# Performance work log

Measured on AMD Instinct MI355X. Metric: run time of the kernel, lower is better.

## Reference

```python
import jax, jax.numpy as jnp
import numpy as np

G, T, H, E, F, C = 8, 2048, 512, 8, 2048, 256


def setup_inputs() -> dict:
    key = jax.random.key(0)
    ks = jax.random.split(key, 4)
    s = 0.02  # truncated-normal stddev in the original init (plain normal here)
    return {
        "x": jax.random.normal(ks[0], (G, T, H), jnp.float32),
        "router_kernel": jax.random.normal(ks[1], (H, E), jnp.float32) * s,
        "router_bias": jnp.zeros((E,), jnp.float32),
        "wi": jax.random.normal(ks[2], (E, H, F), jnp.float32) * s,
        "bi": jnp.zeros((E, F), jnp.float32),
        "wo": jax.random.normal(ks[3], (E, F, H), jnp.float32) * s,
        "bo": jnp.zeros((E, H), jnp.float32),
        "expert_capacity": C,
    }


def reference(x, router_kernel, router_bias, wi, bi, wo, bo, expert_capacity):
    # ---- Router (eval mode: no jitter noise, no dropout) ----
    # logits / probs: [g, t, e]
    router_logits = jnp.einsum("gth,he->gte", x, router_kernel) + router_bias
    router_probs = jax.nn.softmax(router_logits, axis=-1)

    # Experts-choose masked routing: each expert picks its top-capacity tokens.
    probs_et = jnp.swapaxes(router_probs, 1, 2)              # [g, e, t]
    expert_gate, expert_index = jax.lax.top_k(probs_et, expert_capacity)  # [g, e, c]
    dispatch = jax.nn.one_hot(expert_index, x.shape[1], dtype=x.dtype)    # [g, e, c, t]
    combine = dispatch * expert_gate[..., None]                            # [g, e, c, t]

    # ---- Dispatch: gather tokens into per-expert buffers ----
    expert_inputs = jnp.einsum("gect,gth->gech", dispatch, x)  # [g, e, c, h]

    # ---- Per-expert FFN (batched einsum GEMMs) ----
    h_mid = jax.nn.gelu(
        jnp.einsum("gech,ehf->gecf", expert_inputs, wi) + bi[None, :, None, :],
        approximate=False,
    )
    expert_out = jnp.einsum("gecf,efh->gech", h_mid, wo) + bo[None, :, None, :]

    # ---- Combine: scatter expert outputs back, scaled by router prob ----
    y = jnp.einsum("gect,gech->gth", combine, expert_out)  # [g, t, h]
    return y
```

## Files before the change

kernel.cpp:

```cpp
#include <hip/hip_runtime.h>
#include <cstdint>
#include <cstddef>

#define G_ 8
#define T_ 2048
#define H_ 512
#define E_ 8
#define F_ 2048
#define C_ 256

typedef __bf16 bf16x8 __attribute__((ext_vector_type(8)));
typedef float f32x4 __attribute__((ext_vector_type(4)));

__device__ __forceinline__ unsigned short f2bf(float f) {
  unsigned u = __float_as_uint(f);
  u += 0x7FFFu + ((u >> 16) & 1u);
  return (unsigned short)(u >> 16);
}

__device__ __forceinline__ void gload_lds16(const void* g, void* l) {
  __builtin_amdgcn_global_load_lds(
      (const __attribute__((address_space(1))) void*)g,
      (__attribute__((address_space(3))) void*)l, 16, 0, 0);
}

__device__ __forceinline__ float fast_gelu(float v) {
  float z = v * (1.5957691216f + 0.0713540727f * v * v);
  float e = __expf(-z);
  return v * __builtin_amdgcn_rcpf(1.0f + e);
}

#define BARRIER() do { __builtin_amdgcn_s_barrier(); asm volatile("" ::: "memory"); } while (0)

__global__ __launch_bounds__(256) void transconv_kernel(const float* __restrict__ in,
                                 unsigned short* __restrict__ out,
                                 int R, int Cc, int tC) {
  __shared__ float tile[64][65];
  int tid = threadIdx.x;
  int nT = (R / 64) * tC;
  int b = blockIdx.x / nT;
  int rem = blockIdx.x % nT;
  int tr = rem / tC, tc = rem % tC;
  const float* ib = in + (size_t)b * R * Cc + (size_t)(tr * 64) * Cc + tc * 64;
  unsigned short* ob = out + (size_t)b * R * Cc;
  int lr = tid >> 4, lc = (tid & 15) * 4;
#pragma unroll
  for (int i = 0; i < 4; ++i) {
    float4 v = *(const float4*)&ib[(size_t)(lr + 16 * i) * Cc + lc];
    tile[lr + 16 * i][lc + 0] = v.x;
    tile[lr + 16 * i][lc + 1] = v.y;
    tile[lr + 16 * i][lc + 2] = v.z;
    tile[lr + 16 * i][lc + 3] = v.w;
  }
  __syncthreads();
  int r = (tid & 31) * 2, c0 = tid >> 5;
#pragma unroll
  for (int i = 0; i < 8; ++i) {
    int c = c0 + i * 8;
    ushort2 o;
    o.x = f2bf(tile[r][c]);
    o.y = f2bf(tile[r + 1][c]);
    *(ushort2*)&ob[(size_t)(tc * 64 + c) * R + tr * 64 + r] = o;
  }
}

__global__ void router_kernel(const float* __restrict__ x, const float* __restrict__ rk,
                              const float* __restrict__ rb, float* __restrict__ probs) {
  __shared__ float rks[H_ * E_];
  int tid = threadIdx.x;
  for (int i = tid; i < H_ * E_ / 4; i += 256)
    ((float4*)rks)[i] = ((const float4*)rk)[i];
  __syncthreads();
  int wid = tid >> 6, lane = tid & 63;
  int row = blockIdx.x * 4 + wid;
  float acc[E_];
#pragma unroll
  for (int e = 0; e < E_; ++e) acc[e] = 0.f;
  const float* xr = x + (size_t)row * H_;
#pragma unroll
  for (int j = 0; j < H_ / 64; ++j) {
    int h = j * 64 + lane;
    float xv = xr[h];
    const float4* r4 = (const float4*)&rks[h * E_];
    float4 r0 = r4[0], r1 = r4[1];
    acc[0] += xv * r0.x; acc[1] += xv * r0.y; acc[2] += xv * r0.z; acc[3] += xv * r0.w;
    acc[4] += xv * r1.x; acc[5] += xv * r1.y; acc[6] += xv * r1.z; acc[7] += xv * r1.w;
  }
#pragma unroll
  for (int e = 0; e < E_; ++e) {
#pragma unroll
    for (int off = 32; off > 0; off >>= 1) acc[e] += __shfl_xor(acc[e], off);
  }
  float l[E_];
  float mx = -1e30f;
#pragma unroll
  for (int e = 0; e < E_; ++e) { l[e] = acc[e] + rb[e]; mx = fmaxf(mx, l[e]); }
  float s = 0.f;
#pragma unroll
  for (int e = 0; e < E_; ++e) { l[e] = expf(l[e] - mx); s += l[e]; }
  float inv = 1.0f / s;
  int g = row >> 11, t = row & (T_ - 1);
  if (lane < E_) probs[((size_t)(g * E_ + lane)) * T_ + t] = l[lane] * inv;
}

__global__ __launch_bounds__(1024) void topk_kernel(const float* __restrict__ probs,
                                                    int* __restrict__ idx,
                                                    float* __restrict__ gate) {
  __shared__ unsigned long long keys[T_];
  int ge = blockIdx.x, tid = threadIdx.x;
  const float* p = probs + (size_t)ge * T_;
#pragma unroll
  for (int j = 0; j < 2; ++j) {
    int t = tid + j * 1024;
    unsigned pb = __float_as_uint(p[t]);
    keys[t] = ((unsigned long long)pb << 32) | (unsigned)(~t);
  }
  __syncthreads();
  for (unsigned k = 2; k <= T_; k <<= 1) {
    for (unsigned j = k >> 1; j > 0; j >>= 1) {
      unsigned w = tid;
      unsigned i = ((w & ~(j - 1)) << 1) | (w & (j - 1));
      unsigned q = i + j;
      unsigned long long a = keys[i], b = keys[q];
      bool sw = ((i & k) == 0) ? (a < b) : (a > b);
      if (sw) { keys[i] = b; keys[q] = a; }
      __syncthreads();
    }
  }
  if (tid < C_) {
    unsigned long long kk = keys[tid];
    gate[ge * C_ + tid] = __uint_as_float((unsigned)(kk >> 32));
    idx[ge * C_ + tid] = (int)(~(unsigned)kk);
  }
}

__global__ void gather_kernel(const float* __restrict__ x, const int* __restrict__ idx,
                              unsigned short* __restrict__ xin) {
  int tid = threadIdx.x, wid = tid >> 6, lane = tid & 63;
  int r = blockIdx.x * 4 + wid;
  int ge = r >> 8;
  int g = ge >> 3;
  int t = idx[r];
  const float* src = x + ((size_t)(g * T_ + t)) * H_;
  unsigned short* dst = xin + (size_t)r * H_;
#pragma unroll
  for (int j = 0; j < 2; ++j) {
    int h = j * 256 + lane * 4;
    float4 v = *(const float4*)&src[h];
    ushort4 o;
    o.x = f2bf(v.x); o.y = f2bf(v.y); o.z = f2bf(v.z); o.w = f2bf(v.w);
    *(ushort4*)&dst[h] = o;
  }
}

__global__ void build_kernel(const int* __restrict__ idx, int* __restrict__ cnt,
                             unsigned short* __restrict__ ent) {
  int id = blockIdx.x * 256 + threadIdx.x;
  int ge = id >> 8, c = id & 255;
  int g = ge >> 3, e = ge & 7;
  int t = idx[id];
  int pos = atomicAdd(&cnt[g * T_ + t], 1);
  ent[(g * T_ + t) * 8 + pos] = (unsigned short)((e << 8) | c);
}

__global__ __launch_bounds__(256) void combine_kernel(const unsigned short* __restrict__ eout,
                                                      const int* __restrict__ cnt,
                                                      const unsigned short* __restrict__ ent,
                                                      const float* __restrict__ gate,
                                                      float* __restrict__ y) {
  int tid = threadIdx.x, wid = tid >> 6, lane = tid & 63;
  int row = blockIdx.x * 4 + wid;
  int g = row >> 11;
  int n = cnt[row];
  float a[8] = {0.f, 0.f, 0.f, 0.f, 0.f, 0.f, 0.f, 0.f};
  for (int i = 0; i < n; ++i) {
    unsigned pe = ent[row * 8 + i];
    int e = pe >> 8, c = pe & 255;
    int ge = g * E_ + e;
    float gv = gate[ge * C_ + c];
    bf16x8 v = *(const bf16x8*)&eout[((size_t)ge * C_ + c) * H_ + lane * 8];
#pragma unroll
    for (int j = 0; j < 8; ++j) a[j] += gv * (float)v[j];
  }
  float* yr = y + (size_t)row * H_ + lane * 8;
  *(float4*)yr = make_float4(a[0], a[1], a[2], a[3]);
  *(float4*)(yr + 4) = make_float4(a[4], a[5], a[6], a[7]);
}

template<int NT>
__device__ __forceinline__ void gemm_core(const unsigned short* __restrict__ Abase,
                                          const unsigned short* __restrict__ Bbase,
                                          int ldK, unsigned short* lds,
                                          f32x4 (&acc)[8][4]) {
  int tid = threadIdx.x;
  int wid = tid >> 6, lane = tid & 63;
  int l15 = lane & 15, g4 = lane >> 4;
  int wm = wid >> 2, wn = wid & 3;

  int off0, off1;
  {
    int ob = tid * 16;
    int lr = ob >> 7, b = ((ob >> 4) & 7) ^ (lr & 7);
    off0 = (2 * lr + (b >> 2)) * ldK + (b & 3) * 8;
    ob = 8192 + tid * 16;
    lr = ob >> 7; b = ((ob >> 4) & 7) ^ (lr & 7);
    off1 = (2 * lr + (b >> 2)) * ldK + (b & 3) * 8;
  }
  int blkphys = (((l15 & 1) << 2) | g4) ^ (l15 >> 1);
  int abase = (wm * 64 + (l15 >> 1)) * 64 + blkphys * 8;
  int bbase = 8192 + (wn * 32 + (l15 >> 1)) * 64 + blkphys * 8;

  auto stage = [&](int kt) {
    unsigned short* sb = lds + (kt & 3) * 16384;
    const unsigned short* ga = Abase + kt * 32;
    const unsigned short* gb = Bbase + kt * 32;
    gload_lds16(ga + off0, sb + wid * 512);
    gload_lds16(ga + off1, sb + 4096 + wid * 512);
    gload_lds16(gb + off0, sb + 8192 + wid * 512);
    gload_lds16(gb + off1, sb + 12288 + wid * 512);
  };

  auto compute = [&](int kt) {
    const unsigned short* sb = lds + (kt & 3) * 16384;
    bf16x8 af[8], bfr[4];
#pragma unroll
    for (int m = 0; m < 8; ++m) af[m] = *(const bf16x8*)&sb[abase + m * 512];
#pragma unroll
    for (int n = 0; n < 4; ++n) bfr[n] = *(const bf16x8*)&sb[bbase + n * 512];
    __builtin_amdgcn_s_setprio(1);
#pragma unroll
    for (int m = 0; m < 8; ++m)
#pragma unroll
      for (int n = 0; n < 4; ++n)
        acc[m][n] = __builtin_amdgcn_mfma_f32_16x16x32_bf16(af[m], bfr[n], acc[m][n], 0, 0, 0);
    __builtin_amdgcn_s_setprio(0);
  };

  stage(0); stage(1); stage(2);
  asm volatile("s_waitcnt vmcnt(8)" ::: "memory");
  BARRIER();
  for (int kt = 0; kt < NT - 3; ++kt) {
    stage(kt + 3);
    compute(kt);
    asm volatile("s_waitcnt vmcnt(8)" ::: "memory");
    BARRIER();
  }
  compute(NT - 3);
  asm volatile("s_waitcnt vmcnt(4)" ::: "memory");
  BARRIER();
  compute(NT - 2);
  asm volatile("s_waitcnt vmcnt(0)" ::: "memory");
  BARRIER();
  compute(NT - 1);
}

__global__ __launch_bounds__(512, 2) void gemm1_kernel(const unsigned short* __restrict__ xin,
                                                       const unsigned short* __restrict__ wiT,
                                                       const float* __restrict__ bi,
                                                       unsigned short* __restrict__ hmid) {
  __shared__ unsigned short lds[65536];
  int bid = blockIdx.x;
  int swz = (bid & 7) * 64 + (bid >> 3);
  int e = swz >> 6, rem = swz & 63, nt = rem >> 3, g = rem & 7;
  int ge = g * E_ + e;
  const unsigned short* Abase = xin + (size_t)ge * C_ * H_;
  const unsigned short* Bbase = wiT + (size_t)e * F_ * H_ + (size_t)(nt * 256) * H_;
  f32x4 acc[8][4] = {};
  gemm_core<H_ / 32>(Abase, Bbase, H_, lds, acc);

  int tid = threadIdx.x, wid = tid >> 6, lane = tid & 63;
  int l15 = lane & 15, g4 = lane >> 4, wm = wid >> 2, wn = wid & 3;
  unsigned short* Cb = hmid + (size_t)ge * C_ * F_;
  int row0 = wm * 128, col0 = nt * 256 + wn * 64;
#pragma unroll
  for (int m = 0; m < 8; ++m) {
#pragma unroll
    for (int n = 0; n < 4; ++n) {
      int col = col0 + n * 16 + l15;
      float bv = bi[e * F_ + col];
#pragma unroll
      for (int r = 0; r < 4; ++r) {
        int row = row0 + m * 16 + g4 * 4 + r;
        Cb[(size_t)row * F_ + col] = f2bf(fast_gelu(acc[m][n][r] + bv));
      }
    }
  }
}

template<int NT>
__device__ __forceinline__ void gemm2_core(const unsigned short* __restrict__ Abase,
                                           const unsigned short* __restrict__ Bbase,
                                           int ldK, unsigned short* lds,
                                           f32x4 (&acc)[8][4]) {
  int tid = threadIdx.x;
  int wid = tid >> 6, lane = tid & 63;
  int l15 = lane & 15, g4 = lane >> 4;
  int wn = wid;

  auto mkoff = [&](int ob) {
    int lr = ob >> 7, b = ((ob >> 4) & 7) ^ (lr & 7);
    return (2 * lr + (b >> 2)) * ldK + (b & 3) * 8;
  };
  int offA0 = mkoff(tid * 16), offA1 = mkoff(4096 + tid * 16);
  int offB0 = mkoff(tid * 16), offB1 = mkoff(4096 + tid * 16);
  int offB2 = mkoff(8192 + tid * 16), offB3 = mkoff(12288 + tid * 16);

  int blkphys = (((l15 & 1) << 2) | g4) ^ (l15 >> 1);
  int abase = (l15 >> 1) * 64 + blkphys * 8;
  int bbase = 4096 + (wn * 32 + (l15 >> 1)) * 64 + blkphys * 8;

  auto stage = [&](int kt, int slot) {
    unsigned short* sb = lds + slot * 12288;
    const unsigned short* ga = Abase + kt * 32;
    const unsigned short* gb = Bbase + kt * 32;
    gload_lds16(ga + offA0, sb + wid * 512);
    gload_lds16(ga + offA1, sb + 2048 + wid * 512);
    gload_lds16(gb + offB0, sb + 4096 + wid * 512);
    gload_lds16(gb + offB1, sb + 6144 + wid * 512);
    gload_lds16(gb + offB2, sb + 8192 + wid * 512);
    gload_lds16(gb + offB3, sb + 10240 + wid * 512);
  };

  auto compute = [&](int slot) {
    const unsigned short* sb = lds + slot * 12288;
    bf16x8 af[8], bfr[4];
#pragma unroll
    for (int m = 0; m < 8; ++m) af[m] = *(const bf16x8*)&sb[abase + m * 512];
#pragma unroll
    for (int n = 0; n < 4; ++n) bfr[n] = *(const bf16x8*)&sb[bbase + n * 512];
    __builtin_amdgcn_s_setprio(1);
#pragma unroll
    for (int m = 0; m < 8; ++m)
#pragma unroll
      for (int n = 0; n < 4; ++n)
        acc[m][n] = __builtin_amdgcn_mfma_f32_16x16x32_bf16(af[m], bfr[n], acc[m][n], 0, 0, 0);
    __builtin_amdgcn_s_setprio(0);
  };

  stage(0, 0); stage(1, 1);
  asm volatile("s_waitcnt vmcnt(6)" ::: "memory");
  BARRIER();
  int s0 = 0, s1 = 1, s2 = 2;
  for (int kt = 0; kt < NT - 2; ++kt) {
    stage(kt + 2, s2);
    compute(s0);
    asm volatile("s_waitcnt vmcnt(6)" ::: "memory");
    BARRIER();
    int t = s0; s0 = s1; s1 = s2; s2 = t;
  }
  compute(s0);
  asm volatile("s_waitcnt vmcnt(0)" ::: "memory");
  BARRIER();
  compute(s1);
}

__global__ __launch_bounds__(256, 2) void gemm2_kernel(const unsigned short* __restrict__ hmid,
                                                       const unsigned short* __restrict__ woT,
                                                       const float* __restrict__ bo,
                                                       unsigned short* __restrict__ eout) {
  __shared__ unsigned short lds[36864];
  int bid = blockIdx.x;
  int swz = (bid & 7) * 32 + (bid >> 3);
  int e = swz >> 5, rem = swz & 31;
  int tile = rem >> 3, g = rem & 7;
  int tm = tile >> 1, tn = tile & 1;
  int ge = g * E_ + e;
  const unsigned short* Abase = hmid + (size_t)ge * C_ * F_ + (size_t)(tm * 128) * F_;
  const unsigned short* Bbase = woT + (size_t)e * H_ * F_ + (size_t)(tn * 256) * F_;
  f32x4 acc[8][4] = {};
  gemm2_core<F_ / 32>(Abase, Bbase, F_, lds, acc);

  int tid = threadIdx.x, wid = tid >> 6, lane = tid & 63;
  int l15 = lane & 15, g4 = lane >> 4, wn = wid;
  unsigned short* Ob = eout + (size_t)ge * C_ * H_;
  int row0 = tm * 128, col0 = tn * 256 + wn * 64;
#pragma unroll
  for (int m = 0; m < 8; ++m) {
#pragma unroll
    for (int n = 0; n < 4; ++n) {
      int col = col0 + n * 16 + l15;
      float bv = bo[e * H_ + col];
#pragma unroll
      for (int r = 0; r < 4; ++r) {
        int row = row0 + m * 16 + g4 * 4 + r;
        Ob[(size_t)row * H_ + col] = f2bf(acc[m][n][r] + bv);
      }
    }
  }
}

extern "C" void kernel_launch(void* const* d_in, const int* in_sizes, int n_in,
                              void* d_out, int out_size, void* d_ws, size_t ws_size,
                              hipStream_t stream) {
  const float* x  = (const float*)d_in[0];
  const float* rk = (const float*)d_in[1];
  const float* rb = (const float*)d_in[2];
  const float* wi = (const float*)d_in[3];
  const float* bi = (const float*)d_in[4];
  const float* wo = (const float*)d_in[5];
  const float* bo = (const float*)d_in[6];
  float* y = (float*)d_out;

  const size_t WI_T = 0;
  const size_t WO_T = 16777216;
  const size_t PROB = 33554432;
  const size_t IDXO = 34078720;
  const size_t GATO = 34144256;
  const size_t XINO = 34209792;
  const size_t HMID = 50987008;
  const size_t NEED = 118095872;
  if (ws_size < NEED) return;

  char* ws = (char*)d_ws;
  unsigned short* wiT = (unsigned short*)(ws + WI_T);
  unsigned short* woT = (unsigned short*)(ws + WO_T);
  float* probs = (float*)(ws + PROB);
  int* cnt = (int*)(ws + PROB);
  unsigned short* ent = (unsigned short*)(ws + PROB + 65536);
  int* idx = (int*)(ws + IDXO);
  float* gate = (float*)(ws + GATO);
  unsigned short* xin = (unsigned short*)(ws + XINO);
  unsigned short* eout = (unsigned short*)(ws + XINO);
  unsigned short* hmid = (unsigned short*)(ws + HMID);

  transconv_kernel<<<E_ * (H_ / 64) * (F_ / 64), 256, 0, stream>>>(wi, wiT, H_, F_, F_ / 64);
  transconv_kernel<<<E_ * (F_ / 64) * (H_ / 64), 256, 0, stream>>>(wo, woT, F_, H_, H_ / 64);
  router_kernel<<<G_ * T_ / 4, 256, 0, stream>>>(x, rk, rb, probs);
  topk_kernel<<<G_ * E_, 1024, 0, stream>>>(probs, idx, gate);
  hipMemsetAsync(cnt, 0, G_ * T_ * sizeof(int), stream);
  build_kernel<<<G_ * E_ * C_ / 256, 256, 0, stream>>>(idx, cnt, ent);
  gather_kernel<<<G_ * E_ * C_ / 4, 256, 0, stream>>>(x, idx, xin);
  gemm1_kernel<<<512, 512, 0, stream>>>(xin, wiT, bi, hmid);
  gemm2_kernel<<<256, 256, 0, stream>>>(hmid, woT, bo, eout);
  combine_kernel<<<G_ * T_ / 4, 256, 0, stream>>>(eout, cnt, ent, gate, y);
}
```

Before: 167.7 us.

## Fuse prep kernels and split GEMM k-steps into half-tile MFMA phases

Merges the two weight-transpose kernels and the router into one launch, and merges gather with the dispatch-table build into another, which cuts kernel launch and tail overhead. Both GEMM cores now split each k-step into two halves of four M-fragments. The A and B global-to-LDS prefetches are interleaved between the halves, with extra barriers and LDS waits. This is meant to lower register pressure and overlap loads with MFMA, at the cost of more barriers per k-step.

```diff
diff --git a/kernel.cpp b/kernel.cpp
--- a/kernel.cpp
+++ b/kernel.cpp
@@ -31,15 +31,17 @@
 }
 
 #define BARRIER() do { __builtin_amdgcn_s_barrier(); asm volatile("" ::: "memory"); } while (0)
-
-__global__ __launch_bounds__(256) void transconv_kernel(const float* __restrict__ in,
-                                 unsigned short* __restrict__ out,
-                                 int R, int Cc, int tC) {
-  __shared__ float tile[64][65];
+#define WAIT_LDS() do { asm volatile("s_waitcnt lgkmcnt(0)" ::: "memory"); \
+                        __builtin_amdgcn_sched_barrier(0); } while (0)
+
+__device__ __forceinline__ void transconv_body(const float* __restrict__ in,
+                                               unsigned short* __restrict__ out,
+                                               int R, int Cc, int tC, int bidrem,
+                                               float* smem) {
   int tid = threadIdx.x;
   int nT = (R / 64) * tC;
-  int b = blockIdx.x / nT;
-  int rem = blockIdx.x % nT;
+  int b = bidrem / nT;
+  int rem = bidrem % nT;
   int tr = rem / tC, tc = rem % tC;
   const float* ib = in + (size_t)b * R * Cc + (size_t)(tr * 64) * Cc + tc * 64;
   unsigned short* ob = out + (size_t)b * R * Cc;
@@ -47,10 +49,10 @@
 #pragma unroll
   for (int i = 0; i < 4; ++i) {
     float4 v = *(const float4*)&ib[(size_t)(lr + 16 * i) * Cc + lc];
-    tile[lr + 16 * i][lc + 0] = v.x;
-    tile[lr + 16 * i][lc + 1] = v.y;
-    tile[lr + 16 * i][lc + 2] = v.z;
-    tile[lr + 16 * i][lc + 3] = v.w;
+    smem[(lr + 16 * i) * 65 + lc + 0] = v.x;
+    smem[(lr + 16 * i) * 65 + lc + 1] = v.y;
+    smem[(lr + 16 * i) * 65 + lc + 2] = v.z;
+    smem[(lr + 16 * i) * 65 + lc + 3] = v.w;
   }
   __syncthreads();
   int r = (tid & 31) * 2, c0 = tid >> 5;
@@ -58,21 +60,23 @@
   for (int i = 0; i < 8; ++i) {
     int c = c0 + i * 8;
     ushort2 o;
-    o.x = f2bf(tile[r][c]);
-    o.y = f2bf(tile[r + 1][c]);
+    o.x = f2bf(smem[r * 65 + c]);
+    o.y = f2bf(smem[(r + 1) * 65 + c]);
     *(ushort2*)&ob[(size_t)(tc * 64 + c) * R + tr * 64 + r] = o;
   }
 }
 
-__global__ void router_kernel(const float* __restrict__ x, const float* __restrict__ rk,
-                              const float* __restrict__ rb, float* __restrict__ probs) {
-  __shared__ float rks[H_ * E_];
+__device__ __forceinline__ void router_body(const float* __restrict__ x,
+                                            const float* __restrict__ rk,
+                                            const float* __restrict__ rb,
+                                            float* __restrict__ probs,
+                                            int bidrem, float* rks) {
   int tid = threadIdx.x;
   for (int i = tid; i < H_ * E_ / 4; i += 256)
     ((float4*)rks)[i] = ((const float4*)rk)[i];
   __syncthreads();
   int wid = tid >> 6, lane = tid & 63;
-  int row = blockIdx.x * 4 + wid;
+  int row = bidrem * 4 + wid;
   float acc[E_];
 #pragma unroll
   for (int e = 0; e < E_; ++e) acc[e] = 0.f;
@@ -101,6 +105,25 @@
   float inv = 1.0f / s;
   int g = row >> 11, t = row & (T_ - 1);
   if (lane < E_) probs[((size_t)(g * E_ + lane)) * T_ + t] = l[lane] * inv;
+}
+
+__global__ __launch_bounds__(256) void fused1_kernel(const float* __restrict__ wi,
+                                                     unsigned short* __restrict__ wiT,
+                                                     const float* __restrict__ wo,
+                                                     unsigned short* __restrict__ woT,
+                                                     const float* __restrict__ x,
+                                                     const float* __restrict__ rk,
+                                                     const float* __restrict__ rb,
+                                                     float* __restrict__ probs) {
+  __shared__ float smem[64 * 65];
+  int bid = blockIdx.x;
+  if (bid < 2048) {
+    transconv_body(wi, wiT, H_, F_, F_ / 64, bid, smem);
+  } else if (bid < 4096) {
+    transconv_body(wo, woT, F_, H_, H_ / 64, bid - 2048, smem);
+  } else {
+    router_body(x, rk, rb, probs, bid - 4096, smem);
+  }
 }
 
 __global__ __launch_bounds__(1024) void topk_kernel(const float* __restrict__ probs,
@@ -134,33 +157,36 @@
   }
 }
 
-__global__ void gather_kernel(const float* __restrict__ x, const int* __restrict__ idx,
-                              unsigned short* __restrict__ xin) {
-  int tid = threadIdx.x, wid = tid >> 6, lane = tid & 63;
-  int r = blockIdx.x * 4 + wid;
-  int ge = r >> 8;
-  int g = ge >> 3;
-  int t = idx[r];
-  const float* src = x + ((size_t)(g * T_ + t)) * H_;
-  unsigned short* dst = xin + (size_t)r * H_;
-#pragma unroll
-  for (int j = 0; j < 2; ++j) {
-    int h = j * 256 + lane * 4;
-    float4 v = *(const float4*)&src[h];
-    ushort4 o;
-    o.x = f2bf(v.x); o.y = f2bf(v.y); o.z = f2bf(v.z); o.w = f2bf(v.w);
-    *(ushort4*)&dst[h] = o;
-  }
-}
-
-__global__ void build_kernel(const int* __restrict__ idx, int* __restrict__ cnt,
-                             unsigned short* __restrict__ ent) {
-  int id = blockIdx.x * 256 + threadIdx.x;
-  int ge = id >> 8, c = id & 255;
-  int g = ge >> 3, e = ge & 7;
-  int t = idx[id];
-  int pos = atomicAdd(&cnt[g * T_ + t], 1);
-  ent[(g * T_ + t) * 8 + pos] = (unsigned short)((e << 8) | c);
+__global__ __launch_bounds__(256) void fused2_kernel(const float* __restrict__ x,
+                                                     const int* __restrict__ idx,
+                                                     unsigned short* __restrict__ xin,
+                                                     int* __restrict__ cnt,
+                                                     unsigned short* __restrict__ ent) {
+  int bid = blockIdx.x, tid = threadIdx.x;
+  if (bid < 4096) {
+    int wid = tid >> 6, lane = tid & 63;
+    int r = bid * 4 + wid;
+    int ge = r >> 8;
+    int g = ge >> 3;
+    int t = idx[r];
+    const float* src = x + ((size_t)(g * T_ + t)) * H_;
+    unsigned short* dst = xin + (size_t)r * H_;
+#pragma unroll
+    for (int j = 0; j < 2; ++j) {
+      int h = j * 256 + lane * 4;
+      float4 v = *(const float4*)&src[h];
+      ushort4 o;
+      o.x = f2bf(v.x); o.y = f2bf(v.y); o.z = f2bf(v.z); o.w = f2bf(v.w);
+      *(ushort4*)&dst[h] = o;
+    }
+  } else {
+    int id = (bid - 4096) * 256 + tid;
+    int ge = id >> 8, c = id & 255;
+    int g = ge >> 3, e = ge & 7;
+    int t = idx[id];
+    int pos = atomicAdd(&cnt[g * T_ + t], 1);
+    ent[(g * T_ + t) * 8 + pos] = (unsigned short)((e << 8) | c);
+  }
 }
 
 __global__ __launch_bounds__(256) void combine_kernel(const unsigned short* __restrict__ eout,
@@ -210,48 +236,63 @@
   int abase = (wm * 64 + (l15 >> 1)) * 64 + blkphys * 8;
   int bbase = 8192 + (wn * 32 + (l15 >> 1)) * 64 + blkphys * 8;
 
-  auto stage = [&](int kt) {
+  auto stageA = [&](int kt) {
     unsigned short* sb = lds + (kt & 3) * 16384;
     const unsigned short* ga = Abase + kt * 32;
-    const unsigned short* gb = Bbase + kt * 32;
     gload_lds16(ga + off0, sb + wid * 512);
     gload_lds16(ga + off1, sb + 4096 + wid * 512);
+  };
+  auto stageB = [&](int kt) {
+    unsigned short* sb = lds + (kt & 3) * 16384;
+    const unsigned short* gb = Bbase + kt * 32;
     gload_lds16(gb + off0, sb + 8192 + wid * 512);
     gload_lds16(gb + off1, sb + 12288 + wid * 512);
   };
 
-  auto compute = [&](int kt) {
+  bf16x8 bfr[4];
+  auto step = [&](int kt, int prefetch, int vmN) {
     const unsigned short* sb = lds + (kt & 3) * 16384;
-    bf16x8 af[8], bfr[4];
-#pragma unroll
-    for (int m = 0; m < 8; ++m) af[m] = *(const bf16x8*)&sb[abase + m * 512];
+    bf16x8 af[4];
+#pragma unroll
+    for (int m = 0; m < 4; ++m) af[m] = *(const bf16x8*)&sb[abase + m * 512];
 #pragma unroll
     for (int n = 0; n < 4; ++n) bfr[n] = *(const bf16x8*)&sb[bbase + n * 512];
+    if (prefetch) stageA(kt + 3);
+    BARRIER();
+    WAIT_LDS();
     __builtin_amdgcn_s_setprio(1);
 #pragma unroll
-    for (int m = 0; m < 8; ++m)
+    for (int m = 0; m < 4; ++m)
 #pragma unroll
       for (int n = 0; n < 4; ++n)
         acc[m][n] = __builtin_amdgcn_mfma_f32_16x16x32_bf16(af[m], bfr[n], acc[m][n], 0, 0, 0);
     __builtin_amdgcn_s_setprio(0);
-  };
-
-  stage(0); stage(1); stage(2);
+    BARRIER();
+#pragma unroll
+    for (int m = 0; m < 4; ++m) af[m] = *(const bf16x8*)&sb[abase + (4 + m) * 512];
+    if (prefetch) stageB(kt + 3);
+    if (vmN == 8) asm volatile("s_waitcnt vmcnt(8)" ::: "memory");
+    else if (vmN == 4) asm volatile("s_waitcnt vmcnt(4)" ::: "memory");
+    else if (vmN == 0) asm volatile("s_waitcnt vmcnt(0)" ::: "memory");
+    BARRIER();
+    WAIT_LDS();
+    __builtin_amdgcn_s_setprio(1);
+#pragma unroll
+    for (int m = 0; m < 4; ++m)
+#pragma unroll
+      for (int n = 0; n < 4; ++n)
+        acc[4 + m][n] = __builtin_amdgcn_mfma_f32_16x16x32_bf16(af[m], bfr[n], acc[4 + m][n], 0, 0, 0);
+    __builtin_amdgcn_s_setprio(0);
+    BARRIER();
+  };
+
+  stageA(0); stageB(0); stageA(1); stageB(1); stageA(2); stageB(2);
   asm volatile("s_waitcnt vmcnt(8)" ::: "memory");
   BARRIER();
-  for (int kt = 0; kt < NT - 3; ++kt) {
-    stage(kt + 3);
-    compute(kt);
-    asm volatile("s_waitcnt vmcnt(8)" ::: "memory");
-    BARRIER();
-  }
-  compute(NT - 3);
-  asm volatile("s_waitcnt vmcnt(4)" ::: "memory");
-  BARRIER();
-  compute(NT - 2);
-  asm volatile("s_waitcnt vmcnt(0)" ::: "memory");
-  BARRIER();
-  compute(NT - 1);
+  for (int kt = 0; kt < NT - 3; ++kt) step(kt, 1, 8);
+  step(NT - 3, 0, 4);
+  step(NT - 2, 0, 0);
+  step(NT - 1, 0, -1);
 }
 
 __global__ __launch_bounds__(512, 2) void gemm1_kernel(const unsigned short* __restrict__ xin,
@@ -309,49 +350,66 @@
   int abase = (l15 >> 1) * 64 + blkphys * 8;
   int bbase = 4096 + (wn * 32 + (l15 >> 1)) * 64 + blkphys * 8;
 
-  auto stage = [&](int kt, int slot) {
+  auto stageA = [&](int kt, int slot) {
     unsigned short* sb = lds + slot * 12288;
     const unsigned short* ga = Abase + kt * 32;
     const unsigned short* gb = Bbase + kt * 32;
     gload_lds16(ga + offA0, sb + wid * 512);
     gload_lds16(ga + offA1, sb + 2048 + wid * 512);
     gload_lds16(gb + offB0, sb + 4096 + wid * 512);
+  };
+  auto stageB = [&](int kt, int slot) {
+    unsigned short* sb = lds + slot * 12288;
+    const unsigned short* gb = Bbase + kt * 32;
     gload_lds16(gb + offB1, sb + 6144 + wid * 512);
     gload_lds16(gb + offB2, sb + 8192 + wid * 512);
     gload_lds16(gb + offB3, sb + 10240 + wid * 512);
   };
 
-  auto compute = [&](int slot) {
-    const unsigned short* sb = lds + slot * 12288;
-    bf16x8 af[8], bfr[4];
-#pragma unroll
-    for (int m = 0; m < 8; ++m) af[m] = *(const bf16x8*)&sb[abase + m * 512];
+  bf16x8 bfr[4];
+  int s0 = 0, s1 = 1, s2 = 2;
+  auto step = [&](int kt, int prefetch, int vmN) {
+    const unsigned short* sb = lds + s0 * 12288;
+    bf16x8 af[4];
+#pragma unroll
+    for (int m = 0; m < 4; ++m) af[m] = *(const bf16x8*)&sb[abase + m * 512];
 #pragma unroll
     for (int n = 0; n < 4; ++n) bfr[n] = *(const bf16x8*)&sb[bbase + n * 512];
+    if (prefetch) stageA(kt + 2, s2);
+    BARRIER();
+    WAIT_LDS();
     __builtin_amdgcn_s_setprio(1);
 #pragma unroll
-    for (int m = 0; m < 8; ++m)
+    for (int m = 0; m < 4; ++m)
 #pragma unroll
       for (int n = 0; n < 4; ++n)
         acc[m][n] = __builtin_amdgcn_mfma_f32_16x16x32_bf16(af[m], bfr[n], acc[m][n], 0, 0, 0);
     __builtin_amdgcn_s_setprio(0);
-  };
-
-  stage(0, 0); stage(1, 1);
+    BARRIER();
+#pragma unroll
+    for (int m = 0; m < 4; ++m) af[m] = *(const bf16x8*)&sb[abase + (4 + m) * 512];
+    if (prefetch) stageB(kt + 2, s2);
+    if (vmN == 6) asm volatile("s_waitcnt vmcnt(6)" ::: "memory");
+    else if (vmN == 0) asm volatile("s_waitcnt vmcnt(0)" ::: "memory");
+    BARRIER();
+    WAIT_LDS();
+    __builtin_amdgcn_s_setprio(1);
+#pragma unroll
+    for (int m = 0; m < 4; ++m)
+#pragma unroll
+      for (int n = 0; n < 4; ++n)
+        acc[4 + m][n] = __builtin_amdgcn_mfma_f32_16x16x32_bf16(af[m], bfr[n], acc[4 + m][n], 0, 0, 0);
+    __builtin_amdgcn_s_setprio(0);
+    BARRIER();
+    int t = s0; s0 = s1; s1 = s2; s2 = t;
+  };
+
+  stageA(0, 0); stageB(0, 0); stageA(1, 1); stageB(1, 1);
   asm volatile("s_waitcnt vmcnt(6)" ::: "memory");
   BARRIER();
-  int s0 = 0, s1 = 1, s2 = 2;
-  for (int kt = 0; kt < NT - 2; ++kt) {
-    stage(kt + 2, s2);
-    compute(s0);
-    asm volatile("s_waitcnt vmcnt(6)" ::: "memory");
-    BARRIER();
-    int t = s0; s0 = s1; s1 = s2; s2 = t;
-  }
-  compute(s0);
-  asm volatile("s_waitcnt vmcnt(0)" ::: "memory");
-  BARRIER();
-  compute(s1);
+  for (int kt = 0; kt < NT - 2; ++kt) step(kt, 1, 6);
+  step(NT - 2, 0, 0);
+  step(NT - 1, 0, -1);
 }
 
 __global__ __launch_bounds__(256, 2) void gemm2_kernel(const unsigned short* __restrict__ hmid,
@@ -423,13 +481,10 @@
   unsigned short* eout = (unsigned short*)(ws + XINO);
   unsigned short* hmid = (unsigned short*)(ws + HMID);
 
-  transconv_kernel<<<E_ * (H_ / 64) * (F_ / 64), 256, 0, stream>>>(wi, wiT, H_, F_, F_ / 64);
-  transconv_kernel<<<E_ * (F_ / 64) * (H_ / 64), 256, 0, stream>>>(wo, woT, F_, H_, H_ / 64);
-  router_kernel<<<G_ * T_ / 4, 256, 0, stream>>>(x, rk, rb, probs);
+  fused1_kernel<<<8192, 256, 0, stream>>>(wi, wiT, wo, woT, x, rk, rb, probs);
   topk_kernel<<<G_ * E_, 1024, 0, stream>>>(probs, idx, gate);
   hipMemsetAsync(cnt, 0, G_ * T_ * sizeof(int), stream);
-  build_kernel<<<G_ * E_ * C_ / 256, 256, 0, stream>>>(idx, cnt, ent);
-  gather_kernel<<<G_ * E_ * C_ / 4, 256, 0, stream>>>(x, idx, xin);
+  fused2_kernel<<<4096 + 64, 256, 0, stream>>>(x, idx, xin, cnt, ent);
   gemm1_kernel<<<512, 512, 0, stream>>>(xin, wiT, bi, hmid);
   gemm2_kernel<<<256, 256, 0, stream>>>(hmid, woT, bo, eout);
   combine_kernel<<<G_ * T_ / 4, 256, 0, stream>>>(eout, cnt, ent, gate, y);
```

Measured after the change: 161.1 us. 1.04x faster.
